# Optimization experiments

Measured on AMD Instinct MI355X. Metric: run time of the kernel, lower is better.

Reference implementation:

```python
import jax, jax.numpy as jnp
import numpy as np

N_OUT = 4096
N_IN = 4096
NNZ = 1600000
BATCH = 4096


def setup_inputs() -> dict:
    key = jax.random.key(0)
    k1, k2, k3, k4, k5 = jax.random.split(key, 5)
    inputs = jax.random.normal(k1, (N_IN, BATCH), dtype=jnp.float32)
    values = jax.random.normal(k2, (NNZ,), dtype=jnp.float32)
    biases = jax.random.normal(k3, (N_OUT, 1), dtype=jnp.float32)
    rows = jax.random.randint(k4, (NNZ,), 0, N_OUT, dtype=jnp.int32)
    cols = jax.random.randint(k5, (NNZ,), 0, N_IN, dtype=jnp.int32)
    return {"inputs": inputs, "values": values, "biases": biases,
            "rows": rows, "cols": cols}


def reference(inputs, values, biases, rows, cols):
    # torch.sparse.addmm(biases, W_sparse, inputs) with W COO [N_OUT, N_IN].
    # Scatter-add COO entries into a dense weight (duplicates summed, matching
    # coalesce semantics), then one dense GEMM -- avoids an [NNZ, BATCH]
    # gather intermediate while computing identical math.
    W = jnp.zeros((N_OUT, N_IN), dtype=values.dtype).at[rows, cols].add(values)
    out = W @ inputs + biases  # [N_OUT, BATCH], bias broadcast over columns
    return jax.nn.relu(out)    # activation epilogue
```

## Files before the change

### kernel.cpp

```cpp
#include <hip/hip_runtime.h>
#include <stdint.h>

#define N_OUT_  4096
#define N_IN_   4096
#define BATCH_  4096
#define NNZ_    1600000

typedef unsigned short ushort_t;
typedef float  f32x4  __attribute__((ext_vector_type(4)));
typedef short  short8 __attribute__((ext_vector_type(8)));
typedef __bf16 bf16x8 __attribute__((ext_vector_type(8)));

__device__ inline ushort_t f32_to_bf16(float f) {
  uint32_t u = __float_as_uint(f);
  uint32_t r = u + 0x7FFFu + ((u >> 16) & 1u);
  return (ushort_t)(r >> 16);
}
__device__ inline float bf16_to_f32(ushort_t h) {
  return __uint_as_float(((uint32_t)h) << 16);
}

__device__ inline void gload_lds16(const void* g, void* l) {
  __builtin_amdgcn_global_load_lds(
      (const __attribute__((address_space(1))) void*)g,
      (__attribute__((address_space(3))) void*)l,
      16, 0, 0);
}

__device__ inline f32x4 mfma_bf16(short8 a, short8 b, f32x4 c) {
  return __builtin_amdgcn_mfma_f32_16x16x32_bf16(
      __builtin_bit_cast(bf16x8, a), __builtin_bit_cast(bf16x8, b), c, 0, 0, 0);
}

#define BARRIER() asm volatile("s_barrier" ::: "memory")
#define LGKM0()   asm volatile("s_waitcnt lgkmcnt(0)" ::: "memory")
template <int N> __device__ __forceinline__ void waitvm() {
  if constexpr (N == 8)      asm volatile("s_waitcnt vmcnt(8)" ::: "memory");
  else if constexpr (N == 6) asm volatile("s_waitcnt vmcnt(6)" ::: "memory");
  else if constexpr (N == 4) asm volatile("s_waitcnt vmcnt(4)" ::: "memory");
  else                       asm volatile("s_waitcnt vmcnt(0)" ::: "memory");
}

#define SC_BLOCKS2 3125
#define TR_TOTAL 4096
#define FUSED_BLOCKS 7294
#define HALF_NNZ 800000

__device__ inline void cas_add_bf16(uint32_t* __restrict__ W32, int i,
                                    const float* __restrict__ vals,
                                    const int* __restrict__ rows,
                                    const int* __restrict__ cols) {
  const size_t idx =
      (size_t)__builtin_nontemporal_load(rows + i) * N_IN_ +
      __builtin_nontemporal_load(cols + i);
  const float v = __builtin_nontemporal_load(vals + i);
  uint32_t* p = &W32[idx >> 1];
  const bool hi = (idx & 1) != 0;
  uint32_t cur = 0u;
  while (true) {
    ushort_t h = hi ? (ushort_t)(cur >> 16) : (ushort_t)(cur & 0xFFFFu);
    ushort_t nh = f32_to_bf16(bf16_to_f32(h) + v);
    uint32_t nw = hi ? ((cur & 0x0000FFFFu) | ((uint32_t)nh << 16))
                     : ((cur & 0xFFFF0000u) | (uint32_t)nh);
    uint32_t got = atomicCAS(p, cur, nw);
    if (got == cur) break;
    cur = got;
  }
}

__global__ __launch_bounds__(256) void scatter_transpose(
    const float* __restrict__ vals, const int* __restrict__ rows,
    const int* __restrict__ cols, uint32_t* __restrict__ W32,
    const float* __restrict__ in, ushort_t* __restrict__ out) {
  const int b = blockIdx.x;
  const int m = b % 7;
  if (m < 3) {
    const int sb = (b / 7) * 3 + m;
    if (sb >= SC_BLOCKS2) return;
    const int i = sb * 256 + threadIdx.x;
    cas_add_bf16(W32, i, vals, rows, cols);
    cas_add_bf16(W32, i + HALF_NNZ, vals, rows, cols);
  } else {
    const int tb = (b / 7) * 4 + (m - 3);
    if (tb >= TR_TOTAL) return;
    __shared__ float tile[64][65];
    const int bx = (tb & 63) * 64;
    const int by = (tb >> 6) * 64;
    const int t = threadIdx.x;
    const int lr = t >> 4;
    const int lc = (t & 15) * 4;
#pragma unroll
    for (int p = 0; p < 4; ++p) {
      const int i = lr + 16 * p;
      *(float4*)&tile[i][lc] =
          *(const float4*)&in[(size_t)(by + i) * BATCH_ + bx + lc];
    }
    __syncthreads();
    const int s = t & 7;
    const int j0 = t >> 3;
#pragma unroll
    for (int q = 0; q < 2; ++q) {
      const int j = j0 + 32 * q;
      uint32_t w0, w1, w2, w3;
      w0 = (uint32_t)f32_to_bf16(tile[8 * s + 0][j]) |
           ((uint32_t)f32_to_bf16(tile[8 * s + 1][j]) << 16);
      w1 = (uint32_t)f32_to_bf16(tile[8 * s + 2][j]) |
           ((uint32_t)f32_to_bf16(tile[8 * s + 3][j]) << 16);
      w2 = (uint32_t)f32_to_bf16(tile[8 * s + 4][j]) |
           ((uint32_t)f32_to_bf16(tile[8 * s + 5][j]) << 16);
      w3 = (uint32_t)f32_to_bf16(tile[8 * s + 6][j]) |
           ((uint32_t)f32_to_bf16(tile[8 * s + 7][j]) << 16);
      uint4 w = {w0, w1, w2, w3};
      *(uint4*)&out[(size_t)(bx + j) * N_IN_ + by + 8 * s] = w;
    }
  }
}

#define BM 256
#define BN 256
#define BK 32
#define KTILES 128
#define TILE_BYTES 32768
#define B_OFF 16384

__global__ __launch_bounds__(512, 2) void gemm_bias_relu(
    const ushort_t* __restrict__ A,
    const ushort_t* __restrict__ Bt,
    const float* __restrict__ bias,
    float* __restrict__ C) {
  __shared__ __align__(16) char smem[4 * TILE_BYTES];

  const int tid  = threadIdx.x;
  const int wid  = tid >> 6;
  const int lane = tid & 63;

  const int bid = blockIdx.x;
  const int swz = (bid & 7) * 32 + (bid >> 3);
  const int brow = (swz >> 4) * BM;
  const int bcol = (swz & 15) * BN;

  const int wr = wid >> 2;
  const int wc = wid & 3;
  const int fr = lane & 15;
  const int k0slot = lane >> 4;

  int aoff[8], boff[4];
#pragma unroll
  for (int mi = 0; mi < 8; ++mi) {
    int off = (wr * 128 + mi * 16 + fr) * 64 + k0slot * 16;
    aoff[mi] = off ^ (((off >> 7) & 3) << 4);
  }
#pragma unroll
  for (int ni = 0; ni < 4; ++ni) {
    int off = (wc * 64 + ni * 16 + fr) * 64 + k0slot * 16;
    boff[ni] = off ^ (((off >> 7) & 3) << 4);
  }

  const bool isB = wid >= 4;
  const int sw = isB ? wid - 4 : wid;
  const int swzl = lane ^ ((lane >> 3) & 3);
  const int rowInChunk = swzl >> 2;
  const int kelem = (swzl & 3) * 8;
  const ushort_t* gsrc = isB ? Bt : A;
  const size_t laneRowBase =
      (size_t)((isB ? bcol : brow) + sw * 64 + rowInChunk) * N_IN_ + kelem;
  const int ldsOpBase = isB ? B_OFF : 0;

#define STAGE(p, i, t)                                                        \
  gload_lds16(gsrc + laneRowBase + (size_t)(2 * (p) + (i)) * 16 * N_IN_ +     \
                  (size_t)(t) * BK,                                           \
              smem + ((t) & 3) * TILE_BYTES + ldsOpBase +                     \
                  (4 * sw + 2 * (p) + (i)) * 1024)

  f32x4 acc[8][4] = {};
  short8 aF[4], bF[4];

#pragma unroll
  for (int t = 0; t < 3; ++t) {
    STAGE(0, 0, t); STAGE(0, 1, t); STAGE(1, 0, t); STAGE(1, 1, t);
  }
  waitvm<8>();
  BARRIER();

#define TILE(t, S_ON, VM)                                                     \
  do {                                                                        \
    const char* buf = &smem[((t) & 3) * TILE_BYTES];                          \
                                                                 \
    _Pragma("unroll") for (int ni = 0; ni < 4; ++ni)                          \
        bF[ni] = *(const short8*)(buf + B_OFF + boff[ni]);                    \
    _Pragma("unroll") for (int j = 0; j < 4; ++j)                             \
        aF[j] = *(const short8*)(buf + aoff[j]);                              \
    if (S_ON) { STAGE(0, 0, (t) + 3); STAGE(0, 1, (t) + 3); }                 \
    VM;                                                                       \
    BARRIER();                                                                \
    LGKM0();                                                                  \
    __builtin_amdgcn_s_setprio(1);                                            \
    _Pragma("unroll") for (int mi = 0; mi < 4; ++mi)                          \
        _Pragma("unroll") for (int ni = 0; ni < 4; ++ni)                      \
            acc[mi][ni] = mfma_bf16(aF[mi], bF[ni], acc[mi][ni]);             \
    __builtin_amdgcn_s_setprio(0);                                            \
    BARRIER();                                                                \
                                                                 \
    _Pragma("unroll") for (int j = 0; j < 4; ++j)                             \
        aF[j] = *(const short8*)(buf + aoff[j + 4]);                          \
    if (S_ON) { STAGE(1, 0, (t) + 3); STAGE(1, 1, (t) + 3); }                 \
    BARRIER();                                                                \
    LGKM0();                                                                  \
    __builtin_amdgcn_s_setprio(1);                                            \
    _Pragma("unroll") for (int mi = 0; mi < 4; ++mi)                          \
        _Pragma("unroll") for (int ni = 0; ni < 4; ++ni)                      \
            acc[mi + 4][ni] = mfma_bf16(aF[mi], bF[ni], acc[mi + 4][ni]);     \
    __builtin_amdgcn_s_setprio(0);                                            \
    BARRIER();                                                                \
  } while (0)

  for (int t = 0; t < KTILES - 3; ++t) TILE(t, 1, waitvm<6>());
  TILE(KTILES - 3, 0, waitvm<4>());
  TILE(KTILES - 2, 0, waitvm<0>());
  TILE(KTILES - 1, 0, (void)0);

  const int r0 = brow + wr * 128 + k0slot * 4;
  const int c0 = bcol + wc * 64 + fr;
#pragma unroll
  for (int mi = 0; mi < 8; ++mi) {
#pragma unroll
    for (int r = 0; r < 4; ++r) {
      const int row = r0 + mi * 16 + r;
      const float b = bias[row];
#pragma unroll
      for (int ni = 0; ni < 4; ++ni) {
        float v = acc[mi][ni][r] + b;
        C[(size_t)row * BATCH_ + c0 + ni * 16] = v > 0.f ? v : 0.f;
      }
    }
  }
#undef TILE
#undef STAGE
}

extern "C" void kernel_launch(void* const* d_in, const int* in_sizes, int n_in,
                              void* d_out, int out_size, void* d_ws, size_t ws_size,
                              hipStream_t stream) {
  const float* inputs = (const float*)d_in[0];
  const float* values = (const float*)d_in[1];
  const float* biases = (const float*)d_in[2];
  const int*   rows   = (const int*)d_in[3];
  const int*   cols   = (const int*)d_in[4];
  float* out = (float*)d_out;

  const size_t W_BF16_BYTES = (size_t)N_OUT_ * N_IN_ * 2;
  if (ws_size < 2 * W_BF16_BYTES) return;
  char* ws = (char*)d_ws;
  ushort_t* Wb = (ushort_t*)ws;
  ushort_t* Bt = (ushort_t*)(ws + W_BF16_BYTES);

  hipMemsetAsync(Wb, 0, W_BF16_BYTES, stream);
  scatter_transpose<<<FUSED_BLOCKS, 256, 0, stream>>>(
      values, rows, cols, (uint32_t*)Wb, inputs, Bt);
  gemm_bias_relu<<<dim3(256), 512, 0, stream>>>(Wb, Bt, biases, out);
}
```

Before: 192.4 us.

## Switch GEMM to BK=64 double-buffered pipeline with fewer barriers per tile

The GEMM main loop moves from a 4-stage ring of BK=32 tiles with four barriers per tile to a 2-stage double buffer of BK=64 tiles, with one vmcnt(0) wait and one barrier per tile. Each tile now loads all A and B fragments for both k-halves into registers before issuing 64 MFMAs, and the LDS swizzle is rewritten for 128-byte rows. The goal is to cut barrier and synchronization overhead and lengthen the MFMA bursts. In exchange, prefetch depth drops to a single tile, so global-load latency may be exposed, and keeping more fragments live raises register pressure under launch_bounds(512,2).

```diff
diff --git a/kernel.cpp b/kernel.cpp
--- a/kernel.cpp
+++ b/kernel.cpp
@@ -33,12 +33,8 @@
 }
 
 #define BARRIER() asm volatile("s_barrier" ::: "memory")
-#define LGKM0()   asm volatile("s_waitcnt lgkmcnt(0)" ::: "memory")
-template <int N> __device__ __forceinline__ void waitvm() {
-  if constexpr (N == 8)      asm volatile("s_waitcnt vmcnt(8)" ::: "memory");
-  else if constexpr (N == 6) asm volatile("s_waitcnt vmcnt(6)" ::: "memory");
-  else if constexpr (N == 4) asm volatile("s_waitcnt vmcnt(4)" ::: "memory");
-  else                       asm volatile("s_waitcnt vmcnt(0)" ::: "memory");
+__device__ __forceinline__ void waitvm0() {
+  asm volatile("s_waitcnt vmcnt(0)" ::: "memory");
 }
 
 #define SC_BLOCKS2 3125
@@ -118,17 +114,17 @@
 
 #define BM 256
 #define BN 256
-#define BK 32
-#define KTILES 128
-#define TILE_BYTES 32768
-#define B_OFF 16384
+#define BK 64
+#define KTILES 64
+#define BUF_BYTES 65536
+#define B_OFF_L 32768
 
 __global__ __launch_bounds__(512, 2) void gemm_bias_relu(
     const ushort_t* __restrict__ A,
     const ushort_t* __restrict__ Bt,
     const float* __restrict__ bias,
     float* __restrict__ C) {
-  __shared__ __align__(16) char smem[4 * TILE_BYTES];
+  __shared__ __align__(16) char smem[2 * BUF_BYTES];
 
   const int tid  = threadIdx.x;
   const int wid  = tid >> 6;
@@ -144,80 +140,75 @@
   const int fr = lane & 15;
   const int k0slot = lane >> 4;
 
-  int aoff[8], boff[4];
-#pragma unroll
-  for (int mi = 0; mi < 8; ++mi) {
-    int off = (wr * 128 + mi * 16 + fr) * 64 + k0slot * 16;
-    aoff[mi] = off ^ (((off >> 7) & 3) << 4);
-  }
-#pragma unroll
-  for (int ni = 0; ni < 4; ++ni) {
-    int off = (wc * 64 + ni * 16 + fr) * 64 + k0slot * 16;
-    boff[ni] = off ^ (((off >> 7) & 3) << 4);
-  }
+  int aoff[16], boff[8];
+#pragma unroll
+  for (int mi = 0; mi < 8; ++mi)
+#pragma unroll
+    for (int ku = 0; ku < 2; ++ku) {
+      int off = (wr * 128 + mi * 16 + fr) * 128 + ku * 64 + k0slot * 16;
+      aoff[mi * 2 + ku] = off ^ (((off >> 7) & 7) << 4);
+    }
+#pragma unroll
+  for (int ni = 0; ni < 4; ++ni)
+#pragma unroll
+    for (int ku = 0; ku < 2; ++ku) {
+      int off = (wc * 64 + ni * 16 + fr) * 128 + ku * 64 + k0slot * 16;
+      boff[ni * 2 + ku] = off ^ (((off >> 7) & 7) << 4);
+    }
 
   const bool isB = wid >= 4;
   const int sw = isB ? wid - 4 : wid;
-  const int swzl = lane ^ ((lane >> 3) & 3);
-  const int rowInChunk = swzl >> 2;
-  const int kelem = (swzl & 3) * 8;
+  const int l3 = lane >> 3;
+  const int kslot = (lane & 7) ^ l3;
   const ushort_t* gsrc = isB ? Bt : A;
   const size_t laneRowBase =
-      (size_t)((isB ? bcol : brow) + sw * 64 + rowInChunk) * N_IN_ + kelem;
-  const int ldsOpBase = isB ? B_OFF : 0;
-
-#define STAGE(p, i, t)                                                        \
-  gload_lds16(gsrc + laneRowBase + (size_t)(2 * (p) + (i)) * 16 * N_IN_ +     \
+      (size_t)((isB ? bcol : brow) + sw * 64 + l3) * N_IN_ + kslot * 8;
+  const int ldsOpBase = isB ? B_OFF_L : 0;
+
+#define STAGE(j, t)                                                           \
+  gload_lds16(gsrc + laneRowBase + (size_t)(j) * 8 * N_IN_ +                  \
                   (size_t)(t) * BK,                                           \
-              smem + ((t) & 3) * TILE_BYTES + ldsOpBase +                     \
-                  (4 * sw + 2 * (p) + (i)) * 1024)
+              smem + ((t) & 1) * BUF_BYTES + ldsOpBase + (sw * 8 + (j)) * 1024)
 
   f32x4 acc[8][4] = {};
-  short8 aF[4], bF[4];
-
-#pragma unroll
-  for (int t = 0; t < 3; ++t) {
-    STAGE(0, 0, t); STAGE(0, 1, t); STAGE(1, 0, t); STAGE(1, 1, t);
-  }
-  waitvm<8>();
+  short8 a0[8], b0[4], a1[8], b1[4];
+
+#pragma unroll
+  for (int j = 0; j < 8; ++j) STAGE(j, 0);
+  waitvm0();
   BARRIER();
 
-#define TILE(t, S_ON, VM)                                                     \
+#define TILE(t, S_ON)                                                         \
   do {                                                                        \
-    const char* buf = &smem[((t) & 3) * TILE_BYTES];                          \
-                                                                 \
+    const char* buf = &smem[((t) & 1) * BUF_BYTES];                           \
     _Pragma("unroll") for (int ni = 0; ni < 4; ++ni)                          \
-        bF[ni] = *(const short8*)(buf + B_OFF + boff[ni]);                    \
-    _Pragma("unroll") for (int j = 0; j < 4; ++j)                             \
-        aF[j] = *(const short8*)(buf + aoff[j]);                              \
-    if (S_ON) { STAGE(0, 0, (t) + 3); STAGE(0, 1, (t) + 3); }                 \
-    VM;                                                                       \
-    BARRIER();                                                                \
-    LGKM0();                                                                  \
+        b0[ni] = *(const short8*)(buf + B_OFF_L + boff[ni * 2]);              \
+    _Pragma("unroll") for (int mi = 0; mi < 8; ++mi)                          \
+        a0[mi] = *(const short8*)(buf + aoff[mi * 2]);                        \
+    if (S_ON) { STAGE(0, (t) + 1); STAGE(1, (t) + 1);                         \
+                STAGE(2, (t) + 1); STAGE(3, (t) + 1); }                       \
+    _Pragma("unroll") for (int ni = 0; ni < 4; ++ni)                          \
+        b1[ni] = *(const short8*)(buf + B_OFF_L + boff[ni * 2 + 1]);          \
+    _Pragma("unroll") for (int mi = 0; mi < 8; ++mi)                          \
+        a1[mi] = *(const short8*)(buf + aoff[mi * 2 + 1]);                    \
+    if (S_ON) { STAGE(4, (t) + 1); STAGE(5, (t) + 1);                         \
+                STAGE(6, (t) + 1); STAGE(7, (t) + 1); }                       \
     __builtin_amdgcn_s_setprio(1);                                            \
-    _Pragma("unroll") for (int mi = 0; mi < 4; ++mi)                          \
+    _Pragma("unroll") for (int mi = 0; mi < 8; ++mi)                          \
         _Pragma("unroll") for (int ni = 0; ni < 4; ++ni)                      \
-            acc[mi][ni] = mfma_bf16(aF[mi], bF[ni], acc[mi][ni]);             \
+            acc[mi][ni] = mfma_bf16(a0[mi], b0[ni], acc[mi][ni]);             \
     __builtin_amdgcn_s_setprio(0);                                            \
-    BARRIER();                                                                \
-                                                                 \
-    _Pragma("unroll") for (int j = 0; j < 4; ++j)                             \
-        aF[j] = *(const short8*)(buf + aoff[j + 4]);                          \
-    if (S_ON) { STAGE(1, 0, (t) + 3); STAGE(1, 1, (t) + 3); }                 \
-    BARRIER();                                                                \
-    LGKM0();                                                                  \
     __builtin_amdgcn_s_setprio(1);                                            \
-    _Pragma("unroll") for (int mi = 0; mi < 4; ++mi)                          \
+    _Pragma("unroll") for (int mi = 0; mi < 8; ++mi)                          \
         _Pragma("unroll") for (int ni = 0; ni < 4; ++ni)                      \
-            acc[mi + 4][ni] = mfma_bf16(aF[mi], bF[ni], acc[mi + 4][ni]);     \
+            acc[mi][ni] = mfma_bf16(a1[mi], b1[ni], acc[mi][ni]);             \
     __builtin_amdgcn_s_setprio(0);                                            \
+    waitvm0();                                                                \
     BARRIER();                                                                \
   } while (0)
 
-  for (int t = 0; t < KTILES - 3; ++t) TILE(t, 1, waitvm<6>());
-  TILE(KTILES - 3, 0, waitvm<4>());
-  TILE(KTILES - 2, 0, waitvm<0>());
-  TILE(KTILES - 1, 0, (void)0);
+  for (int t = 0; t < KTILES - 1; ++t) TILE(t, 1);
+  TILE(KTILES - 1, 0);
 
   const int r0 = brow + wr * 128 + k0slot * 4;
   const int c0 = bcol + wc * 64 + fr;
```

After: 201.8 us. +4.9%, slower.
